# Optimization experiments

Measured on AMD Instinct MI355X. Metric: run time of the kernel, lower is better.

Reference implementation:

```python
import jax, jax.numpy as jnp
import numpy as np

N, E, P = 20000, 320000, 100000
TC, HID, H, OUT, PH = 256, 64, 4, 256, 512


def gat_conv(x, src, dst, n, W, a_src, a_dst, b):
    # PyG GATConv (eval, dropout=0): per-head linear, LeakyReLU(0.2) attention,
    # scatter-softmax over incoming edges, scatter-add aggregation, concat heads + bias.
    Hh, C = a_src.shape
    h = (x @ W).reshape(n, Hh, C)
    alpha_src = (h * a_src).sum(-1)  # [N, H]
    alpha_dst = (h * a_dst).sum(-1)  # [N, H]
    e = jax.nn.leaky_relu(alpha_src[src] + alpha_dst[dst], 0.2)  # [E, H]
    emax = jax.ops.segment_max(e, dst, num_segments=n)
    emax = jnp.where(jnp.isfinite(emax), emax, 0.0)
    p = jnp.exp(e - emax[dst])
    denom = jax.ops.segment_sum(p, dst, num_segments=n)
    alpha = p / jnp.maximum(denom[dst], 1e-16)  # [E, H]
    out = jax.ops.segment_sum(h[src] * alpha[:, :, None], dst, num_segments=n)  # [N, H, C]
    return out.reshape(n, Hh * C) + b


def setup_inputs() -> dict:
    key = jax.random.key(0)
    ks = jax.random.split(key, 24)
    s = 0.05
    inp = {
        "x": jax.random.normal(ks[0], (N, TC), jnp.float32),
        "edge_index": jax.random.randint(ks[1], (2, E), 0, N, jnp.int64),
        "u_nodes": jax.random.randint(ks[2], (P,), 0, N, jnp.int64),
        "v_nodes": jax.random.randint(ks[3], (P,), 0, N, jnp.int64),
        # GATConv 1: in=TC, out=HID per head, heads=H, concat
        "W1": jax.random.normal(ks[4], (TC, H * HID), jnp.float32) * s,
        "a1s": jax.random.normal(ks[5], (H, HID), jnp.float32) * s,
        "a1d": jax.random.normal(ks[6], (H, HID), jnp.float32) * s,
        "b1": jax.random.normal(ks[7], (H * HID,), jnp.float32) * s,
        # GATConv 2: in=H*HID, out=OUT, heads=1
        "W2": jax.random.normal(ks[8], (H * HID, OUT), jnp.float32) * s,
        "a2s": jax.random.normal(ks[9], (1, OUT), jnp.float32) * s,
        "a2d": jax.random.normal(ks[10], (1, OUT), jnp.float32) * s,
        "b2": jax.random.normal(ks[11], (OUT,), jnp.float32) * s,
        # gate MLP: (TC+OUT) -> (TC+OUT)//2 -> 1, Sigmoid
        "gw1": jax.random.normal(ks[12], (TC + OUT, (TC + OUT) // 2), jnp.float32) * s,
        "gb1": jax.random.normal(ks[13], ((TC + OUT) // 2,), jnp.float32) * s,
        "gw2": jax.random.normal(ks[14], ((TC + OUT) // 2, 1), jnp.float32) * s,
        "gb2": jax.random.normal(ks[15], (1,), jnp.float32) * s,
        # predictor: 2*OUT -> PH -> 1 (dropout is identity in eval)
        "pw1": jax.random.normal(ks[16], (2 * OUT, PH), jnp.float32) * s,
        "pb1": jax.random.normal(ks[17], (PH,), jnp.float32) * s,
        "pw2": jax.random.normal(ks[18], (PH, 1), jnp.float32) * s,
        "pb2": jax.random.normal(ks[19], (1,), jnp.float32) * s,
    }
    return inp


def reference(x, edge_index, u_nodes, v_nodes, W1, a1s, a1d, b1, W2, a2s, a2d, b2,
              gw1, gb1, gw2, gb2, pw1, pb1, pw2, pb2):
    n = x.shape[0]
    loops = jnp.arange(n, dtype=edge_index.dtype)
    src = jnp.concatenate([edge_index[0], loops])  # PyG GATConv adds self-loops
    dst = jnp.concatenate([edge_index[1], loops])
    h = jax.nn.elu(gat_conv(x, src, dst, n, W1, a1s, a1d, b1))
    h_graph = gat_conv(h, src, dst, n, W2, a2s, a2d, b2)
    gate_in = jnp.concatenate([x, h_graph], axis=-1)
    g = jax.nn.sigmoid(jax.nn.relu(gate_in @ gw1 + gb1) @ gw2 + gb2)  # [N,1]
    h_final = (1.0 - g) * x + g * h_graph
    pair = jnp.concatenate([h_final[u_nodes], h_final[v_nodes]], axis=-1)  # [P, 2*OUT]
    out = jax.nn.relu(pair @ pw1 + pb1) @ pw2 + pb2
    return out.squeeze(-1)
```

## Files before the change

kernel.cpp:

```cpp
#include <hip/hip_runtime.h>
#include <math.h>

#define N_NODES 20000
#define N_EDGES 320000
#define EPRIME  (N_EDGES + N_NODES)
#define NP      100000

typedef __bf16 bf16x8 __attribute__((ext_vector_type(8)));
typedef float  f32x4  __attribute__((ext_vector_type(4)));

__device__ __forceinline__ float b2f(unsigned short u) {
    union { float f; unsigned int v; } x; x.v = ((unsigned int)u) << 16; return x.f;
}
__device__ __forceinline__ unsigned short f2b(float f) {
    union { float f; unsigned int v; } x; x.f = f;
    unsigned int r = (x.v + 0x7fffu + ((x.v >> 16) & 1u)) >> 16;
    return (unsigned short)r;
}
__device__ __forceinline__ float lrelu02(float v) { return v > 0.0f ? v : 0.2f * v; }

__device__ __forceinline__ void gload16(const void* g, void* l) {
    __builtin_amdgcn_global_load_lds(
        (const __attribute__((address_space(1))) void*)g,
        (__attribute__((address_space(3))) void*)l, 16, 0, 0);
}

template<int BM, int ASRC, int EPI>
__global__ __launch_bounds__(256) void mgemm_k(
    const unsigned short* __restrict__ A0, const unsigned short* __restrict__ A1,
    const unsigned short* __restrict__ BT,
    const float* __restrict__ bias, const float* __restrict__ w2,
    unsigned short* __restrict__ Cb, float* __restrict__ outp,
    int M, int K, int Nn)
{
    constexpr int NJA   = BM / 64;
    constexpr int MF    = BM / 32;
    constexpr int WROWS = BM / 2;

    __shared__ unsigned short As[2][BM * 32];
    __shared__ unsigned short Bs[2][4096];

    const int tid = threadIdx.x;
    const int wave = tid >> 6, lane = tid & 63;
    const int row0 = blockIdx.x * BM, col0 = blockIdx.y * 128;
    const int ksub = (((lane & 3) ^ ((lane >> 3) & 3)) * 8);

    const unsigned short* aL[NJA];
    const unsigned short* aH[NJA];
    const unsigned short* bP[2];
    #pragma unroll
    for (int j = 0; j < NJA; ++j) {
        const int r = j * 64 + wave * 16 + (lane >> 2);
        int ar = row0 + r; if (ar > M - 1) ar = M - 1;
        if (ASRC == 0) { aL[j] = A0 + (long)ar * K;  aH[j] = aL[j]; }
        else           { aL[j] = A0 + (long)ar * 256; aH[j] = A1 + (long)ar * 256; }
    }
    #pragma unroll
    for (int j = 0; j < 2; ++j) {
        const int r = j * 64 + wave * 16 + (lane >> 2);
        bP[j] = BT + (long)(col0 + r) * K;
    }

    const int wm = wave >> 1, wn = wave & 1;
    const int lrow = lane & 15;
    const int lks = ((((lane >> 4) ^ ((lane >> 1) & 3)) & 3) * 8);

    f32x4 acc[MF][4] = {};

    const int nT = K >> 5;
    int buf = 0;

    auto stage = [&](int bi, int t) {
        const int k0 = t << 5;
        #pragma unroll
        for (int j = 0; j < NJA; ++j) {
            const unsigned short* ga;
            if (ASRC == 0) ga = aL[j] + k0 + ksub;
            else ga = (k0 < 256) ? (aL[j] + k0 + ksub) : (aH[j] + (k0 - 256) + ksub);
            const int ci = j * 256 + wave * 64 + lane;
            gload16(ga, &As[bi][ci * 8]);
        }
        #pragma unroll
        for (int j = 0; j < 2; ++j) {
            const int ci = j * 256 + wave * 64 + lane;
            gload16(bP[j] + k0 + ksub, &Bs[bi][ci * 8]);
        }
    };

    stage(0, 0);
    __syncthreads();
    for (int t = 0; t < nT; ++t) {
        if (t + 1 < nT) stage(buf ^ 1, t + 1);
        bf16x8 a[MF], b[4];
        #pragma unroll
        for (int i = 0; i < MF; ++i)
            a[i] = *(const bf16x8*)&As[buf][(wm * WROWS + i * 16 + lrow) * 32 + lks];
        #pragma unroll
        for (int j = 0; j < 4; ++j)
            b[j] = *(const bf16x8*)&Bs[buf][(wn * 64 + j * 16 + lrow) * 32 + lks];
        #pragma unroll
        for (int i = 0; i < MF; ++i)
            #pragma unroll
            for (int j = 0; j < 4; ++j)
                acc[i][j] = __builtin_amdgcn_mfma_f32_16x16x32_bf16(a[i], b[j], acc[i][j], 0, 0, 0);
        __syncthreads();
        buf ^= 1;
    }

    if constexpr (EPI == 0 || EPI == 1) {
        #pragma unroll
        for (int i = 0; i < MF; ++i) {
            #pragma unroll
            for (int p = 0; p < 4; ++p) {
                const int row = row0 + wm * WROWS + i * 16 + (lane >> 4) * 4 + p;
                if (row < M) {
                    #pragma unroll
                    for (int j = 0; j < 4; ++j) {
                        const int col = col0 + wn * 64 + j * 16 + (lane & 15);
                        float v = acc[i][j][p];
                        if (EPI == 1) { v += bias[col]; v = v > 0.f ? v : 0.f; }
                        Cb[(long)row * Nn + col] = f2b(v);
                    }
                }
            }
        }
    } else {
        float s[MF][4];
        #pragma unroll
        for (int i = 0; i < MF; ++i) {
            #pragma unroll
            for (int p = 0; p < 4; ++p) {
                float t = 0.f;
                #pragma unroll
                for (int j = 0; j < 4; ++j) {
                    const int col = col0 + wn * 64 + j * 16 + (lane & 15);
                    float v = acc[i][j][p] + bias[col];
                    v = v > 0.f ? v : 0.f;
                    t += v * w2[col];
                }
                s[i][p] = t;
            }
        }
        #pragma unroll
        for (int off = 1; off < 16; off <<= 1) {
            #pragma unroll
            for (int i = 0; i < MF; ++i)
                #pragma unroll
                for (int p = 0; p < 4; ++p)
                    s[i][p] += __shfl_xor(s[i][p], off);
        }
        if ((lane & 15) == 0) {
            #pragma unroll
            for (int i = 0; i < MF; ++i)
                #pragma unroll
                for (int p = 0; p < 4; ++p) {
                    const int row = row0 + wm * WROWS + i * 16 + (lane >> 4) * 4 + p;
                    if (row < M) atomicAdd(outp + row, s[i][p]);
                }
        }
    }
}

__global__ __launch_bounds__(512) void zgemm_k(
    const unsigned short* __restrict__ A0,
    const unsigned short* __restrict__ BT,
    const float* __restrict__ bias,
    unsigned short* __restrict__ Cb,
    int M)
{
    __shared__ unsigned short As[2][4096];
    __shared__ unsigned short Bs[2][8192];

    const int tid = threadIdx.x;
    const int wave = tid >> 6, lane = tid & 63;
    const int row0 = blockIdx.x * 128, col0 = blockIdx.y * 256;
    const int ksub = (((tid & 3) ^ ((tid >> 3) & 3)) * 8);

    const unsigned short* aP;
    {
        int ar = row0 + (tid >> 2); if (ar > M - 1) ar = M - 1;
        aP = A0 + (long)ar * 256;
    }
    const unsigned short* bP[2];
    #pragma unroll
    for (int j = 0; j < 2; ++j)
        bP[j] = BT + (long)(col0 + j * 128 + (tid >> 2)) * 256;

    const int wm = wave >> 2, wn = wave & 3;
    const int lrow = lane & 15;
    const int lks = ((((lane >> 4) ^ ((lane >> 1) & 3)) & 3) * 8);

    f32x4 acc[4][4] = {};
    int buf = 0;

    auto stage = [&](int bi, int t) {
        const int k0 = t << 5;
        gload16(aP + k0 + ksub, &As[bi][tid * 8]);
        #pragma unroll
        for (int j = 0; j < 2; ++j)
            gload16(bP[j] + k0 + ksub, &Bs[bi][(j * 512 + tid) * 8]);
    };

    stage(0, 0);
    __syncthreads();
    #pragma unroll
    for (int t = 0; t < 8; ++t) {
        if (t + 1 < 8) stage(buf ^ 1, t + 1);
        bf16x8 a[4], b[4];
        #pragma unroll
        for (int i = 0; i < 4; ++i)
            a[i] = *(const bf16x8*)&As[buf][(wm * 64 + i * 16 + lrow) * 32 + lks];
        #pragma unroll
        for (int j = 0; j < 4; ++j)
            b[j] = *(const bf16x8*)&Bs[buf][(wn * 64 + j * 16 + lrow) * 32 + lks];
        #pragma unroll
        for (int i = 0; i < 4; ++i)
            #pragma unroll
            for (int j = 0; j < 4; ++j)
                acc[i][j] = __builtin_amdgcn_mfma_f32_16x16x32_bf16(a[i], b[j], acc[i][j], 0, 0, 0);
        __syncthreads();
        buf ^= 1;
    }

    #pragma unroll
    for (int i = 0; i < 4; ++i) {
        #pragma unroll
        for (int p = 0; p < 4; ++p) {
            const int row = row0 + wm * 64 + i * 16 + (lane >> 4) * 4 + p;
            if (row < M) {
                #pragma unroll
                for (int j = 0; j < 4; ++j) {
                    const int col = col0 + wn * 64 + j * 16 + (lane & 15);
                    float v = acc[i][j][p];
                    if (col < 512) v += bias[col];
                    Cb[(long)row * 1024 + col] = f2b(v);
                }
            }
        }
    }
}

__global__ __launch_bounds__(256) void pair_k(
    const unsigned short* __restrict__ Z, const int* __restrict__ un,
    const int* __restrict__ vn, const float* __restrict__ pw2,
    const float* __restrict__ pb2, float* __restrict__ out)
{
    const int wv = threadIdx.x >> 6, lane = threadIdx.x & 63;
    const int p = blockIdx.x * 4 + wv;
    if (p >= NP) return;
    const int u = un[p], v = vn[p];
    const int c0 = lane * 8;
    const uint4 zu = *(const uint4*)&Z[(long)u * 1024 + c0];
    const uint4 zv = *(const uint4*)&Z[(long)v * 1024 + 512 + c0];
    const float4 w2a = *(const float4*)&pw2[c0];
    const float4 w2b = *(const float4*)&pw2[c0 + 4];

    float zt[8], zb[8];
    zt[0] = b2f(zu.x & 0xffff); zt[1] = b2f(zu.x >> 16);
    zt[2] = b2f(zu.y & 0xffff); zt[3] = b2f(zu.y >> 16);
    zt[4] = b2f(zu.z & 0xffff); zt[5] = b2f(zu.z >> 16);
    zt[6] = b2f(zu.w & 0xffff); zt[7] = b2f(zu.w >> 16);
    zb[0] = b2f(zv.x & 0xffff); zb[1] = b2f(zv.x >> 16);
    zb[2] = b2f(zv.y & 0xffff); zb[3] = b2f(zv.y >> 16);
    zb[4] = b2f(zv.z & 0xffff); zb[5] = b2f(zv.z >> 16);
    zb[6] = b2f(zv.w & 0xffff); zb[7] = b2f(zv.w >> 16);

    const float ww[8] = {w2a.x, w2a.y, w2a.z, w2a.w, w2b.x, w2b.y, w2b.z, w2b.w};
    float s = 0.f;
    #pragma unroll
    for (int q = 0; q < 8; ++q) {
        float t = zt[q] + zb[q];
        t = t > 0.f ? t : 0.f;
        s = fmaf(t, ww[q], s);
    }
    #pragma unroll
    for (int off = 1; off < 64; off <<= 1) s += __shfl_xor(s, off);
    if (lane == 0) out[p] = s + pb2[0];
}

__global__ __launch_bounds__(256) void prep_k(
    const float* __restrict__ x, unsigned short* __restrict__ xb,
    const float* __restrict__ W1, unsigned short* __restrict__ W1t,
    const float* __restrict__ W2, unsigned short* __restrict__ W2t,
    const float* __restrict__ gw1, unsigned short* __restrict__ gw1t,
    const float* __restrict__ pw1, unsigned short* __restrict__ pw1t2,
    int* __restrict__ deg, float* __restrict__ gacc)
{
    const int bid = blockIdx.x, tid = threadIdx.x;
    if (bid < 5000) {
        const int id = bid * 256 + tid;
        const float4 v = ((const float4*)x)[id];
        ushort4 o;
        o.x = f2b(v.x); o.y = f2b(v.y); o.z = f2b(v.z); o.w = f2b(v.w);
        ((ushort4*)xb)[id] = o;
    } else if (bid < 5256) {
        const int id = (bid - 5000) * 256 + tid;
        W1t[(id & 255) * 256 + (id >> 8)] = f2b(W1[id]);
    } else if (bid < 5512) {
        const int id = (bid - 5256) * 256 + tid;
        W2t[(id & 255) * 256 + (id >> 8)] = f2b(W2[id]);
    } else if (bid < 6024) {
        const int id = (bid - 5512) * 256 + tid;
        gw1t[(id & 255) * 512 + (id >> 8)] = f2b(gw1[id]);
    } else if (bid < 7048) {
        const int id = (bid - 6024) * 256 + tid;
        const int r = id >> 9, c = id & 511;
        const int j = (r < 256) ? c : (512 + c);
        const int k = (r < 256) ? r : (r - 256);
        pw1t2[j * 256 + k] = f2b(pw1[id]);
    } else if (bid < 7127) {
        const int i = (bid - 7048) * 256 + tid;
        if (i < N_NODES) deg[i] = 1;
    } else {
        const int i = (bid - 7127) * 256 + tid;
        if (i < N_NODES) gacc[i] = 0.f;
    }
}

__global__ __launch_bounds__(256) void alpha1_k(
    const unsigned short* __restrict__ h1, const float* __restrict__ a1s,
    const float* __restrict__ a1d, float* __restrict__ as1, float* __restrict__ ad1)
{
    const int wid = threadIdx.x >> 6;
    const int lane = threadIdx.x & 63;
    const int n = blockIdx.x * 4 + wid;
    if (n >= N_NODES) return;
    float ps[4], pd[4];
    #pragma unroll
    for (int h = 0; h < 4; ++h) {
        const float hv = b2f(h1[(long)n * 256 + h * 64 + lane]);
        ps[h] = hv * a1s[h * 64 + lane];
        pd[h] = hv * a1d[h * 64 + lane];
    }
    #pragma unroll
    for (int off = 32; off > 0; off >>= 1) {
        #pragma unroll
        for (int h = 0; h < 4; ++h) {
            ps[h] += __shfl_xor(ps[h], off);
            pd[h] += __shfl_xor(pd[h], off);
        }
    }
    if (lane == 0) {
        #pragma unroll
        for (int h = 0; h < 4; ++h) {
            as1[n * 4 + h] = ps[h];
            ad1[n * 4 + h] = pd[h];
        }
    }
}

__global__ __launch_bounds__(256) void alpha2_k(
    const unsigned short* __restrict__ h2, const float* __restrict__ a2s,
    const float* __restrict__ a2d, float* __restrict__ as2, float* __restrict__ ad2)
{
    const int wid = threadIdx.x >> 6;
    const int lane = threadIdx.x & 63;
    const int n = blockIdx.x * 4 + wid;
    if (n >= N_NODES) return;
    float ps = 0.f, pd = 0.f;
    #pragma unroll
    for (int q = 0; q < 4; ++q) {
        const float hv = b2f(h2[(long)n * 256 + q * 64 + lane]);
        ps += hv * a2s[q * 64 + lane];
        pd += hv * a2d[q * 64 + lane];
    }
    #pragma unroll
    for (int off = 32; off > 0; off >>= 1) {
        ps += __shfl_xor(ps, off);
        pd += __shfl_xor(pd, off);
    }
    if (lane == 0) { as2[n] = ps; ad2[n] = pd; }
}

__global__ __launch_bounds__(256) void deg_count_k(const int* __restrict__ ei, int* __restrict__ deg)
{
    const int e = blockIdx.x * 256 + threadIdx.x;
    if (e < N_EDGES) atomicAdd(&deg[ei[N_EDGES + e]], 1);
}

__global__ __launch_bounds__(1024) void scan_k(const int* __restrict__ deg,
                                               int* __restrict__ indptr,
                                               int* __restrict__ pos)
{
    __shared__ int sums[1024];
    const int tid = threadIdx.x;
    const int CH = 20;
    const int start = tid * CH;
    const int end = min(start + CH, N_NODES);
    int s = 0;
    for (int i = start; i < end; ++i) s += deg[i];
    sums[tid] = s;
    __syncthreads();
    for (int off = 1; off < 1024; off <<= 1) {
        const int v = sums[tid];
        const int add = (tid >= off) ? sums[tid - off] : 0;
        __syncthreads();
        sums[tid] = v + add;
        __syncthreads();
    }
    int pre = sums[tid] - s;
    for (int i = start; i < end; ++i) {
        indptr[i] = pre;
        pos[i] = pre;
        pre += deg[i];
    }
    if (tid == 1023) indptr[N_NODES] = sums[1023];
}

__global__ __launch_bounds__(256) void fill_k(const int* __restrict__ ei,
                                              int* __restrict__ pos, int* __restrict__ csr)
{
    const int i = blockIdx.x * 256 + threadIdx.x;
    if (i < N_EDGES) {
        const int s = ei[i], d = ei[N_EDGES + i];
        const int p = atomicAdd(&pos[d], 1);
        csr[p] = s;
    } else if (i < EPRIME) {
        const int n = i - N_EDGES;
        const int p = atomicAdd(&pos[n], 1);
        csr[p] = n;
    }
}

__global__ __launch_bounds__(256) void agg1_k(
    const unsigned short* __restrict__ h1, const float* __restrict__ as1,
    const float* __restrict__ ad1, const int* __restrict__ indptr,
    const int* __restrict__ csr, const float* __restrict__ b1,
    unsigned short* __restrict__ out)
{
    __shared__ int   ssrc[4][64];
    __shared__ float sp[4][64 * 4];
    const int wv = threadIdx.x >> 6, lane = threadIdx.x & 63;
    const int n = blockIdx.x * 4 + wv;
    if (n >= N_NODES) return;

    const int beg = indptr[n], end = indptr[n + 1];
    const float4 ad = ((const float4*)ad1)[n];
    const int c0 = lane * 4;
    const int hd = lane >> 4;

    float acc[4] = {0.f, 0.f, 0.f, 0.f};
    float psum[4] = {0.f, 0.f, 0.f, 0.f};

    for (int base = beg; base < end; base += 64) {
        const int cnt = min(64, end - base);
        if (lane < cnt) {
            const int s = csr[base + lane];
            const float4 av = ((const float4*)as1)[s];
            float4 p;
            p.x = __expf(lrelu02(av.x + ad.x));
            p.y = __expf(lrelu02(av.y + ad.y));
            p.z = __expf(lrelu02(av.z + ad.z));
            p.w = __expf(lrelu02(av.w + ad.w));
            ssrc[wv][lane] = s;
            *(float4*)&sp[wv][lane * 4] = p;
            psum[0] += p.x; psum[1] += p.y; psum[2] += p.z; psum[3] += p.w;
        }
        asm volatile("s_waitcnt lgkmcnt(0)" ::: "memory");
        __builtin_amdgcn_sched_barrier(0);
        for (int e = 0; e < cnt; ++e) {
            const int s = ssrc[wv][e];
            const float w = sp[wv][e * 4 + hd];
            const ushort4 hv = *(const ushort4*)&h1[(long)s * 256 + c0];
            acc[0] = fmaf(w, b2f(hv.x), acc[0]);
            acc[1] = fmaf(w, b2f(hv.y), acc[1]);
            acc[2] = fmaf(w, b2f(hv.z), acc[2]);
            acc[3] = fmaf(w, b2f(hv.w), acc[3]);
        }
        __builtin_amdgcn_sched_barrier(0);
        __builtin_amdgcn_wave_barrier();
    }

    #pragma unroll
    for (int off = 1; off < 64; off <<= 1) {
        #pragma unroll
        for (int h = 0; h < 4; ++h) psum[h] += __shfl_xor(psum[h], off);
    }
    const float invd = 1.0f / psum[hd];

    ushort4 o;
    float v;
    v = acc[0] * invd + b1[c0 + 0]; o.x = f2b(v > 0.f ? v : (__expf(v) - 1.0f));
    v = acc[1] * invd + b1[c0 + 1]; o.y = f2b(v > 0.f ? v : (__expf(v) - 1.0f));
    v = acc[2] * invd + b1[c0 + 2]; o.z = f2b(v > 0.f ? v : (__expf(v) - 1.0f));
    v = acc[3] * invd + b1[c0 + 3]; o.w = f2b(v > 0.f ? v : (__expf(v) - 1.0f));
    *(ushort4*)&out[(long)n * 256 + c0] = o;
}

__global__ __launch_bounds__(256) void agg2_k(
    const unsigned short* __restrict__ h2, const float* __restrict__ as2,
    const float* __restrict__ ad2, const int* __restrict__ indptr,
    const int* __restrict__ csr, const float* __restrict__ b2,
    unsigned short* __restrict__ outb)
{
    __shared__ int   ssrc[4][64];
    __shared__ float sp[4][64];
    const int wv = threadIdx.x >> 6, lane = threadIdx.x & 63;
    const int n = blockIdx.x * 4 + wv;
    if (n >= N_NODES) return;

    const int beg = indptr[n], end = indptr[n + 1];
    const float adv = ad2[n];
    const int c0 = lane * 4;

    float acc[4] = {0.f, 0.f, 0.f, 0.f};
    float psum = 0.f;

    for (int base = beg; base < end; base += 64) {
        const int cnt = min(64, end - base);
        if (lane < cnt) {
            const int s = csr[base + lane];
            const float p = __expf(lrelu02(as2[s] + adv));
            ssrc[wv][lane] = s;
            sp[wv][lane] = p;
            psum += p;
        }
        asm volatile("s_waitcnt lgkmcnt(0)" ::: "memory");
        __builtin_amdgcn_sched_barrier(0);
        for (int e = 0; e < cnt; ++e) {
            const int s = ssrc[wv][e];
            const float w = sp[wv][e];
            const ushort4 hv = *(const ushort4*)&h2[(long)s * 256 + c0];
            acc[0] = fmaf(w, b2f(hv.x), acc[0]);
            acc[1] = fmaf(w, b2f(hv.y), acc[1]);
            acc[2] = fmaf(w, b2f(hv.z), acc[2]);
            acc[3] = fmaf(w, b2f(hv.w), acc[3]);
        }
        __builtin_amdgcn_sched_barrier(0);
        __builtin_amdgcn_wave_barrier();
    }

    #pragma unroll
    for (int off = 1; off < 64; off <<= 1) psum += __shfl_xor(psum, off);
    const float invd = 1.0f / psum;

    ushort4 o;
    o.x = f2b(acc[0] * invd + b2[c0 + 0]);
    o.y = f2b(acc[1] * invd + b2[c0 + 1]);
    o.z = f2b(acc[2] * invd + b2[c0 + 2]);
    o.w = f2b(acc[3] * invd + b2[c0 + 3]);
    *(ushort4*)&outb[(long)n * 256 + c0] = o;
}

__global__ __launch_bounds__(256) void gatefin2_k(
    const float* __restrict__ gacc, const float* __restrict__ gb2,
    const float* __restrict__ x, const unsigned short* __restrict__ hgb,
    unsigned short* __restrict__ hfb)
{
    const int wid = threadIdx.x >> 6;
    const int lane = threadIdx.x & 63;
    const int n = blockIdx.x * 4 + wid;
    if (n >= N_NODES) return;
    const float g = 1.0f / (1.0f + __expf(-(gacc[n] + gb2[0])));
    #pragma unroll
    for (int q = 0; q < 4; ++q) {
        const int c = q * 64 + lane;
        const float xv = x[(long)n * 256 + c];
        const float hv = b2f(hgb[(long)n * 256 + c]);
        hfb[(long)n * 256 + c] = f2b((1.0f - g) * xv + g * hv);
    }
}

extern "C" void kernel_launch(void* const* d_in, const int* in_sizes, int n_in,
                              void* d_out, int out_size, void* d_ws, size_t ws_size,
                              hipStream_t stream)
{
    const float* x   = (const float*)d_in[0];
    const int*   ei  = (const int*)d_in[1];
    const int*   un  = (const int*)d_in[2];
    const int*   vn  = (const int*)d_in[3];
    const float* W1  = (const float*)d_in[4];
    const float* a1s = (const float*)d_in[5];
    const float* a1d = (const float*)d_in[6];
    const float* b1  = (const float*)d_in[7];
    const float* W2  = (const float*)d_in[8];
    const float* a2s = (const float*)d_in[9];
    const float* a2d = (const float*)d_in[10];
    const float* b2  = (const float*)d_in[11];
    const float* gw1 = (const float*)d_in[12];
    const float* gb1 = (const float*)d_in[13];
    const float* gw2 = (const float*)d_in[14];
    const float* gb2 = (const float*)d_in[15];
    const float* pw1 = (const float*)d_in[16];
    const float* pb1 = (const float*)d_in[17];
    const float* pw2 = (const float*)d_in[18];
    const float* pb2 = (const float*)d_in[19];
    float* out = (float*)d_out;

    dim3 b256(256);

    if (ws_size < 58720256u) return;

    unsigned short* Z     = (unsigned short*)d_ws;
    unsigned short* bufHb = Z;
    unsigned short* hgb   = Z + 5120000;
    unsigned short* xb    = Z + 10240000;
    unsigned short* hfb   = Z + 20480000;
    unsigned short* W1t   = hfb + 5120000;
    unsigned short* W2t   = W1t + 65536;
    unsigned short* gw1t  = W2t + 65536;
    unsigned short* pw1t2 = gw1t + 131072;
    float* as1v = (float*)(pw1t2 + 262144);
    float* ad1v = as1v + 80000;
    float* as2v = ad1v + 80000;
    float* ad2v = as2v + 20000;
    int* deg    = (int*)(ad2v + 20000);
    int* indptr = deg + 20000;
    int* pos    = indptr + 20032;
    int* csr    = pos + 20000;
    float* gacc = (float*)(csr + EPRIME);

    prep_k<<<7206, b256, 0, stream>>>(x, xb, W1, W1t, W2, W2t, gw1, gw1t,
                                      pw1, pw1t2, deg, gacc);
    deg_count_k<<<(N_EDGES + 255) / 256, b256, 0, stream>>>(ei, deg);
    scan_k<<<1, 1024, 0, stream>>>(deg, indptr, pos);
    fill_k<<<(EPRIME + 255) / 256, b256, 0, stream>>>(ei, pos, csr);

    mgemm_k<64, 0, 0><<<dim3(313, 2), b256, 0, stream>>>(
        xb, nullptr, W1t, nullptr, nullptr, bufHb, nullptr, N_NODES, 256, 256);
    alpha1_k<<<5000, b256, 0, stream>>>(bufHb, a1s, a1d, as1v, ad1v);
    agg1_k<<<5000, b256, 0, stream>>>(bufHb, as1v, ad1v, indptr, csr, b1, hfb);

    mgemm_k<64, 0, 0><<<dim3(313, 2), b256, 0, stream>>>(
        hfb, nullptr, W2t, nullptr, nullptr, bufHb, nullptr, N_NODES, 256, 256);
    alpha2_k<<<5000, b256, 0, stream>>>(bufHb, a2s, a2d, as2v, ad2v);
    agg2_k<<<5000, b256, 0, stream>>>(bufHb, as2v, ad2v, indptr, csr, b2, hgb);

    mgemm_k<64, 1, 2><<<dim3(313, 2), b256, 0, stream>>>(
        xb, hgb, gw1t, gb1, gw2, nullptr, gacc, N_NODES, 512, 256);
    gatefin2_k<<<5000, b256, 0, stream>>>(gacc, gb2, x, hgb, hfb);

    zgemm_k<<<dim3(157, 4), dim3(512), 0, stream>>>(hfb, pw1t2, pb1, Z, N_NODES);

    pair_k<<<25000, b256, 0, stream>>>(Z, un, vn, pw2, pb2, out);
}
```

Measured before the change: 247.8 us.

## Load full-K tiles into LDS once in zgemm and shrink the N tile

The zgemm kernel now loads the entire 128x256 A tile and a 128x256 B tile into LDS in one pass with an XOR swizzle, then runs all eight K steps with no further barriers. This replaces the double-buffered 32-wide K staging. The N tile is halved to 128 columns, so the grid doubles to 8 column blocks and each wave keeps 4x2 accumulators instead of 4x4. The aim is to remove per-step synchronisation and lower register pressure. In exchange it uses 128 KB of LDS per block, which limits occupancy to one block per CU, gives up load/compute overlap, and re-reads A twice as often.

```diff
diff --git a/kernel.cpp b/kernel.cpp
--- a/kernel.cpp
+++ b/kernel.cpp
@@ -168,69 +168,59 @@
     unsigned short* __restrict__ Cb,
     int M)
 {
-    __shared__ unsigned short As[2][4096];
-    __shared__ unsigned short Bs[2][8192];
+    __shared__ unsigned short As[128 * 256];
+    __shared__ unsigned short Bs[128 * 256];
 
     const int tid = threadIdx.x;
     const int wave = tid >> 6, lane = tid & 63;
-    const int row0 = blockIdx.x * 128, col0 = blockIdx.y * 256;
-    const int ksub = (((tid & 3) ^ ((tid >> 3) & 3)) * 8);
-
-    const unsigned short* aP;
-    {
-        int ar = row0 + (tid >> 2); if (ar > M - 1) ar = M - 1;
-        aP = A0 + (long)ar * 256;
-    }
-    const unsigned short* bP[2];
-    #pragma unroll
-    for (int j = 0; j < 2; ++j)
-        bP[j] = BT + (long)(col0 + j * 128 + (tid >> 2)) * 256;
+    const int row0 = blockIdx.x * 128, col0 = blockIdx.y * 128;
+
+    const int srcC = ((tid & 31) ^ ((tid >> 5) & 7)) * 8;
+    const int rb = tid >> 5;
+    #pragma unroll
+    for (int i = 0; i < 8; ++i) {
+        const int r = rb + i * 16;
+        int ar = row0 + r; if (ar > M - 1) ar = M - 1;
+        gload16(A0 + (long)ar * 256 + srcC, &As[(i * 512 + tid) * 8]);
+        gload16(BT + (long)(col0 + r) * 256 + srcC, &Bs[(i * 512 + tid) * 8]);
+    }
+    __syncthreads();
 
     const int wm = wave >> 2, wn = wave & 3;
-    const int lrow = lane & 15;
-    const int lks = ((((lane >> 4) ^ ((lane >> 1) & 3)) & 3) * 8);
-
-    f32x4 acc[4][4] = {};
-    int buf = 0;
-
-    auto stage = [&](int bi, int t) {
-        const int k0 = t << 5;
-        gload16(aP + k0 + ksub, &As[bi][tid * 8]);
-        #pragma unroll
-        for (int j = 0; j < 2; ++j)
-            gload16(bP[j] + k0 + ksub, &Bs[bi][(j * 512 + tid) * 8]);
-    };
-
-    stage(0, 0);
-    __syncthreads();
+    const int lrow = lane & 15, g = lane >> 4;
+    const int rx = lrow & 7;
+
+    f32x4 acc[4][2] = {};
     #pragma unroll
     for (int t = 0; t < 8; ++t) {
-        if (t + 1 < 8) stage(buf ^ 1, t + 1);
-        bf16x8 a[4], b[4];
-        #pragma unroll
-        for (int i = 0; i < 4; ++i)
-            a[i] = *(const bf16x8*)&As[buf][(wm * 64 + i * 16 + lrow) * 32 + lks];
-        #pragma unroll
-        for (int j = 0; j < 4; ++j)
-            b[j] = *(const bf16x8*)&Bs[buf][(wn * 64 + j * 16 + lrow) * 32 + lks];
+        bf16x8 a[4], b[2];
+        const int slot = ((t * 4 + g) ^ rx) * 8;
+        #pragma unroll
+        for (int i = 0; i < 4; ++i) {
+            const int row = wm * 64 + i * 16 + lrow;
+            a[i] = *(const bf16x8*)&As[row * 256 + slot];
+        }
+        #pragma unroll
+        for (int j = 0; j < 2; ++j) {
+            const int row = wn * 32 + j * 16 + lrow;
+            b[j] = *(const bf16x8*)&Bs[row * 256 + slot];
+        }
         #pragma unroll
         for (int i = 0; i < 4; ++i)
             #pragma unroll
-            for (int j = 0; j < 4; ++j)
+            for (int j = 0; j < 2; ++j)
                 acc[i][j] = __builtin_amdgcn_mfma_f32_16x16x32_bf16(a[i], b[j], acc[i][j], 0, 0, 0);
-        __syncthreads();
-        buf ^= 1;
     }
 
     #pragma unroll
     for (int i = 0; i < 4; ++i) {
         #pragma unroll
         for (int p = 0; p < 4; ++p) {
-            const int row = row0 + wm * 64 + i * 16 + (lane >> 4) * 4 + p;
+            const int row = row0 + wm * 64 + i * 16 + g * 4 + p;
             if (row < M) {
                 #pragma unroll
-                for (int j = 0; j < 4; ++j) {
-                    const int col = col0 + wn * 64 + j * 16 + (lane & 15);
+                for (int j = 0; j < 2; ++j) {
+                    const int col = col0 + wn * 32 + j * 16 + lrow;
                     float v = acc[i][j][p];
                     if (col < 512) v += bias[col];
                     Cb[(long)row * 1024 + col] = f2b(v);
@@ -630,7 +620,7 @@
         xb, hgb, gw1t, gb1, gw2, nullptr, gacc, N_NODES, 512, 256);
     gatefin2_k<<<5000, b256, 0, stream>>>(gacc, gb2, x, hgb, hfb);
 
-    zgemm_k<<<dim3(157, 4), dim3(512), 0, stream>>>(hfb, pw1t2, pb1, Z, N_NODES);
+    zgemm_k<<<dim3(157, 8), dim3(512), 0, stream>>>(hfb, pw1t2, pb1, Z, N_NODES);
 
     pair_k<<<25000, b256, 0, stream>>>(Z, un, vn, pw2, pb2, out);
 }
```

After: 263.3 us. 6.2% more time.

## Load zgemm MFMA operands directly from global memory instead of LDS staging

Applied to the files above, without the earlier changes.

The Z-projection GEMM drops its double-buffered LDS staging (global_load_lds plus barriers) and has each wave load its bf16x8 A and B fragments straight from global memory into registers. The block shrinks to 64 rows by 256 columns with 256 threads, and the grid doubles in the row dimension. This removes LDS traffic and __syncthreads overhead and raises block count. In exchange there is less data reuse across waves, since each wave refetches the A rows, and no software prefetch, so it relies on L1/L2 caching and latency hiding.

```diff
diff --git a/kernel.cpp b/kernel.cpp
--- a/kernel.cpp
+++ b/kernel.cpp
@@ -161,76 +161,54 @@
     }
 }
 
-__global__ __launch_bounds__(512) void zgemm_k(
+__global__ __launch_bounds__(256) void zgemm_k(
     const unsigned short* __restrict__ A0,
     const unsigned short* __restrict__ BT,
     const float* __restrict__ bias,
     unsigned short* __restrict__ Cb,
     int M)
 {
-    __shared__ unsigned short As[2][4096];
-    __shared__ unsigned short Bs[2][8192];
-
-    const int tid = threadIdx.x;
-    const int wave = tid >> 6, lane = tid & 63;
-    const int row0 = blockIdx.x * 128, col0 = blockIdx.y * 256;
-    const int ksub = (((tid & 3) ^ ((tid >> 3) & 3)) * 8);
-
-    const unsigned short* aP;
-    {
-        int ar = row0 + (tid >> 2); if (ar > M - 1) ar = M - 1;
-        aP = A0 + (long)ar * 256;
-    }
-    const unsigned short* bP[2];
-    #pragma unroll
-    for (int j = 0; j < 2; ++j)
-        bP[j] = BT + (long)(col0 + j * 128 + (tid >> 2)) * 256;
-
-    const int wm = wave >> 2, wn = wave & 3;
-    const int lrow = lane & 15;
-    const int lks = ((((lane >> 4) ^ ((lane >> 1) & 3)) & 3) * 8);
+    const int wave = threadIdx.x >> 6, lane = threadIdx.x & 63;
+    const int row0 = blockIdx.x * 64;
+    const int col0 = blockIdx.y * 256 + wave * 64;
+    const int lr = lane & 15, lk = (lane >> 4) * 8;
+
+    const unsigned short* aP[4];
+    #pragma unroll
+    for (int i = 0; i < 4; ++i) {
+        int ar = row0 + i * 16 + lr; if (ar > M - 1) ar = M - 1;
+        aP[i] = A0 + (long)ar * 256 + lk;
+    }
+    const unsigned short* bP[4];
+    #pragma unroll
+    for (int j = 0; j < 4; ++j)
+        bP[j] = BT + (long)(col0 + j * 16 + lr) * 256 + lk;
 
     f32x4 acc[4][4] = {};
-    int buf = 0;
-
-    auto stage = [&](int bi, int t) {
-        const int k0 = t << 5;
-        gload16(aP + k0 + ksub, &As[bi][tid * 8]);
-        #pragma unroll
-        for (int j = 0; j < 2; ++j)
-            gload16(bP[j] + k0 + ksub, &Bs[bi][(j * 512 + tid) * 8]);
-    };
-
-    stage(0, 0);
-    __syncthreads();
     #pragma unroll
     for (int t = 0; t < 8; ++t) {
-        if (t + 1 < 8) stage(buf ^ 1, t + 1);
+        const int k0 = t * 32;
         bf16x8 a[4], b[4];
         #pragma unroll
-        for (int i = 0; i < 4; ++i)
-            a[i] = *(const bf16x8*)&As[buf][(wm * 64 + i * 16 + lrow) * 32 + lks];
-        #pragma unroll
-        for (int j = 0; j < 4; ++j)
-            b[j] = *(const bf16x8*)&Bs[buf][(wn * 64 + j * 16 + lrow) * 32 + lks];
+        for (int i = 0; i < 4; ++i) a[i] = *(const bf16x8*)(aP[i] + k0);
+        #pragma unroll
+        for (int j = 0; j < 4; ++j) b[j] = *(const bf16x8*)(bP[j] + k0);
         #pragma unroll
         for (int i = 0; i < 4; ++i)
             #pragma unroll
             for (int j = 0; j < 4; ++j)
                 acc[i][j] = __builtin_amdgcn_mfma_f32_16x16x32_bf16(a[i], b[j], acc[i][j], 0, 0, 0);
-        __syncthreads();
-        buf ^= 1;
     }
 
     #pragma unroll
     for (int i = 0; i < 4; ++i) {
         #pragma unroll
         for (int p = 0; p < 4; ++p) {
-            const int row = row0 + wm * 64 + i * 16 + (lane >> 4) * 4 + p;
+            const int row = row0 + i * 16 + (lane >> 4) * 4 + p;
             if (row < M) {
                 #pragma unroll
                 for (int j = 0; j < 4; ++j) {
-                    const int col = col0 + wn * 64 + j * 16 + (lane & 15);
+                    const int col = col0 + j * 16 + lr;
                     float v = acc[i][j][p];
                     if (col < 512) v += bias[col];
                     Cb[(long)row * 1024 + col] = f2b(v);
@@ -630,7 +608,7 @@
         xb, hgb, gw1t, gb1, gw2, nullptr, gacc, N_NODES, 512, 256);
     gatefin2_k<<<5000, b256, 0, stream>>>(gacc, gb2, x, hgb, hfb);
 
-    zgemm_k<<<dim3(157, 4), dim3(512), 0, stream>>>(hfb, pw1t2, pb1, Z, N_NODES);
+    zgemm_k<<<dim3(313, 4), b256, 0, stream>>>(hfb, pw1t2, pb1, Z, N_NODES);
 
     pair_k<<<25000, b256, 0, stream>>>(Z, un, vn, pw2, pb2, out);
 }
```

New measurement: 278.4 us. 12.3% more time.
